# Kernel tuning notes

Measured on AMD Instinct MI355X. Metric: run time of the kernel, lower is better.

## Reference

```python
import jax, jax.numpy as jnp
import numpy as np

K = 16          # nsample / knn k
GROUPS = 4      # GroupNorm groups
EPS = 1e-5


def setup_inputs() -> dict:
    key = jax.random.key(0)
    ks = jax.random.split(key, 10)
    B, N = 8, 2048
    x = jax.random.normal(ks[0], (B, 3, N), jnp.float32)
    f = x  # at first call features == coordinates
    w = lambda i, shape: jax.random.normal(ks[i], shape, jnp.float32) * 0.05
    return dict(
        x=x, f=f,
        # input_trans: Conv1d(3 -> 64)
        W_it=w(1, (64, 3)), b_it=jnp.zeros((64,), jnp.float32),
        # layer1: Conv2d(128 -> 128, bias=False) + GroupNorm(4, 128)
        W1=w(2, (128, 128)), gn_g=jnp.ones((128,), jnp.float32), gn_b=jnp.zeros((128,), jnp.float32),
        # mlp1: Conv2d(128->256), Conv2d(256->512)
        Wa=w(3, (256, 128)), ba=jnp.zeros((256,), jnp.float32),
        Wb=w(4, (512, 256)), bb=jnp.zeros((512,), jnp.float32),
        # mlp2: Conv1d(640->256), Conv1d(256->128)
        Wc=w(5, (256, 640)), bc=jnp.zeros((256,), jnp.float32),
        Wd=w(6, (128, 256)), bd=jnp.zeros((128,), jnp.float32),
        # mlp3: Conv1d(128->256), Conv1d(256->512)
        We=w(7, (256, 128)), be=jnp.zeros((256,), jnp.float32),
        Wf=w(8, (512, 256)), bf=jnp.zeros((512,), jnp.float32),
    )


def _knn_idx(x):
    # x: (B, 3, N) -> idx: (B, N, K) indices of K nearest neighbors (self-knn)
    coor = jnp.transpose(x, (0, 2, 1))                       # (B, N, 3)
    sq = jnp.sum(coor * coor, axis=-1)                        # (B, N)
    d = sq[:, :, None] + sq[:, None, :] - 2.0 * jnp.einsum('bnc,bmc->bnm', coor, coor)
    _, idx = jax.lax.top_k(-d, K)                             # smallest distances
    return idx


def _group_norm(y, gamma, beta):
    # y: (B, N, K, C); torch GroupNorm normalizes over (C/g, N, K) per (b, group)
    B, N, Kk, C = y.shape
    yg = y.reshape(B, N, Kk, GROUPS, C // GROUPS)
    mu = jnp.mean(yg, axis=(1, 2, 4), keepdims=True)
    var = jnp.var(yg, axis=(1, 2, 4), keepdims=True)
    yg = (yg - mu) * jax.lax.rsqrt(var + EPS)
    return yg.reshape(B, N, Kk, C) * gamma + beta


def reference(x, f, W_it, b_it, W1, gn_g, gn_b, Wa, ba, Wb, bb, Wc, bc, Wd, bd, We, be, Wf, bf):
    B, _, N = x.shape
    idx = _knn_idx(x)                                          # (B, N, K)

    # input_trans: 1x1 conv over channels, channels-last layout (B, N, C)
    h = jnp.einsum('bcn,oc->bno', f, W_it) + b_it              # (B, N, 64)

    # graph feature: gather neighbors, build [nb - h, h]
    nb = jax.vmap(lambda hb, ib: hb[ib])(h, idx)               # (B, N, K, 64)
    hq = h[:, :, None, :]                                       # (B, N, 1, 64)
    feat = jnp.concatenate([nb - hq, jnp.broadcast_to(hq, nb.shape)], axis=-1)  # (B, N, K, 128)

    # layer1: conv1x1 (no bias) + GroupNorm + LeakyReLU(0.2)
    y = jnp.einsum('bnkc,oc->bnko', feat, W1)                  # (B, N, K, 128)
    y = jax.nn.leaky_relu(_group_norm(y, gn_g, gn_b), 0.2)

    local_base = jnp.max(y, axis=2)                             # (B, N, 128)

    # mlp1 over edges, then max over K and global max over N
    g = jax.nn.relu(jnp.einsum('bnkc,oc->bnko', y, Wa) + ba)    # (B, N, K, 256)
    g = jax.nn.relu(jnp.einsum('bnkc,oc->bnko', g, Wb) + bb)    # (B, N, K, 512)
    gfeat = jnp.max(g, axis=2)                                  # (B, N, 512)
    gmax = jnp.max(gfeat, axis=1, keepdims=True)                # (B, 1, 512)

    cat = jnp.concatenate([local_base, jnp.broadcast_to(gmax, (B, N, 512))], axis=-1)  # (B, N, 640)

    lf = jax.nn.relu(jnp.einsum('bnc,oc->bno', cat, Wc) + bc)   # (B, N, 256)
    lf = jax.nn.relu(jnp.einsum('bnc,oc->bno', lf, Wd) + bd)    # (B, N, 128)

    gl = jax.nn.relu(jnp.einsum('bnc,oc->bno', lf, We) + be)    # (B, N, 256)
    gl = jax.nn.relu(jnp.einsum('bnc,oc->bno', gl, Wf) + bf)    # (B, N, 512)
    gl = jnp.max(gl, axis=1, keepdims=True)                     # (B, 1, 512)

    global_feat = jnp.transpose(gl, (0, 2, 1))                  # (B, 512, 1)
    local_feat = jnp.transpose(lf, (0, 2, 1))                   # (B, 128, N)
    return (global_feat, local_feat)
```

## Files before the change

### kernel.cpp

```cpp
#include <hip/hip_runtime.h>
#include <hip/hip_bf16.h>

#define BATCH 8
#define NPTS 2048
#define KNNK 16
#define CH 64
#define CF 128
#define CA 256
#define CB 512
#define CCAT 640
#define CC 256
#define CD 128
#define CE 256
#define CG 512
#define NGRP 4
#define EPSF 1e-5f
#define GF_OFF (BATCH*CG)
#define P 8
#define MROWS (P*KNNK)
#define TM 64

typedef __attribute__((ext_vector_type(8))) short short8v;
typedef __attribute__((ext_vector_type(4))) float f32x4;

__device__ inline short f2bf(float f) {
  __hip_bfloat16 h = __float2bfloat16(f);
  return *reinterpret_cast<short*>(&h);
}

#define LIDX(r, c, ROW) ((r)*(ROW) + ((c) ^ (((r)&7)<<3)))

__device__ inline void pack_dev(const float* __restrict__ W, short* __restrict__ Wp,
                                int O, int C, int ld, int tid) {
  int KS = C >> 5;
  int total = (O >> 4) * KS * 64;
  if (tid >= total) return;
  int l = tid & 63;
  int fs = tid >> 6;
  int nt = fs / KS, ks = fs - nt * KS;
  int o = nt * 16 + (l & 15);
  int c = ks * 32 + (l >> 4) * 8;
  const float* src = W + (size_t)o * ld + c;
  short8v v;
#pragma unroll
  for (int j = 0; j < 8; ++j) v[j] = f2bf(src[j]);
  *(short8v*)&Wp[(size_t)tid * 8] = v;
}

__global__ __launch_bounds__(256)
void k_prep(const float* __restrict__ f, const float* __restrict__ Wit,
            const float* __restrict__ bit, float* __restrict__ h,
            const float* __restrict__ W1, short* __restrict__ W1p,
            const float* __restrict__ Wa, short* __restrict__ Wap,
            const float* __restrict__ Wb, short* __restrict__ Wbp,
            const float* __restrict__ Wc, short* __restrict__ WcLp,
            const float* __restrict__ Wd, short* __restrict__ Wdp,
            const float* __restrict__ We, short* __restrict__ Wep,
            const float* __restrict__ Wf, short* __restrict__ Wfp) {
  int blk = blockIdx.x;
  if (blk < 4096) {
    int t = blk * 256 + threadIdx.x;
    int o = t & (CH - 1);
    int bn = t >> 6;
    int n = bn & (NPTS - 1);
    int b = bn >> 11;
    float f0 = f[(b*3 + 0)*NPTS + n];
    float f1 = f[(b*3 + 1)*NPTS + n];
    float f2 = f[(b*3 + 2)*NPTS + n];
    h[t] = f0*Wit[o*3+0] + f1*Wit[o*3+1] + f2*Wit[o*3+2] + bit[o];
  } else if (blk < 4104) pack_dev(W1, W1p, CF, CF, CF, (blk-4096)*256 + threadIdx.x);
  else if (blk < 4120) pack_dev(Wa, Wap, CA, CF, CF, (blk-4104)*256 + threadIdx.x);
  else if (blk < 4184) pack_dev(Wb, Wbp, CB, CA, CA, (blk-4120)*256 + threadIdx.x);
  else if (blk < 4200) pack_dev(Wc, WcLp, CC, CF, CCAT, (blk-4184)*256 + threadIdx.x);
  else if (blk < 4216) pack_dev(Wd, Wdp, CD, CC, CC, (blk-4200)*256 + threadIdx.x);
  else if (blk < 4232) pack_dev(We, Wep, CE, CD, CD, (blk-4216)*256 + threadIdx.x);
  else                 pack_dev(Wf, Wfp, CG, CE, CE, (blk-4232)*256 + threadIdx.x);
}

__global__ __launch_bounds__(512)
void k_knn(const float* __restrict__ x, int* __restrict__ idxout) {
  __shared__ float xs0[2112], xs1[2112], xs2[2112], sqs[2112];
  int blk = blockIdx.x;
  int b = blk >> 8;
  int n0 = (blk & 255) * 8;
  int t = threadIdx.x;
  for (int i = t; i < NPTS; i += 512) {
    float x0 = x[(b*3 + 0)*NPTS + i];
    float x1 = x[(b*3 + 1)*NPTS + i];
    float x2 = x[(b*3 + 2)*NPTS + i];
    int a = (i >> 5)*33 + (i & 31);
    xs0[a] = x0; xs1[a] = x1; xs2[a] = x2;
    sqs[a] = __fadd_rn(__fadd_rn(__fmul_rn(x0,x0), __fmul_rn(x1,x1)), __fmul_rn(x2,x2));
  }
  __syncthreads();
  int lane = t & 63, wv = t >> 6;
  int q = n0 + wv;
  int qa = (q >> 5)*33 + (q & 31);
  float qx = xs0[qa], qy = xs1[qa], qz = xs2[qa];
  float sqq = sqs[qa];
  float d[32];
  int base = lane * 32;
#pragma unroll
  for (int jj = 0; jj < 32; ++jj) {
    int a = lane*33 + jj;
    float mx = xs0[a], my = xs1[a], mz = xs2[a];
    float dot = __fadd_rn(__fadd_rn(__fmul_rn(qx,mx), __fmul_rn(qy,my)), __fmul_rn(qz,mz));
    d[jj] = __fsub_rn(__fadd_rn(sqq, sqs[a]), __fadd_rn(dot, dot));
  }
  const float FINF = __builtin_inff();
  float sv0 = d[0]; int si0 = base;
#pragma unroll
  for (int jj = 1; jj < 16; ++jj)
    if (d[jj] < sv0) { sv0 = d[jj]; si0 = base + jj; }
  float sv1 = d[16]; int si1 = base + 16;
#pragma unroll
  for (int jj = 17; jj < 32; ++jj)
    if (d[jj] < sv1) { sv1 = d[jj]; si1 = base + jj; }
  int gsel = 0;
#pragma unroll
  for (int r = 0; r < KNNK; ++r) {
    float v = sv0; int i = si0;
    if (sv1 < v || (sv1 == v && si1 < i)) { v = sv1; i = si1; }
#pragma unroll
    for (int off = 32; off > 0; off >>= 1) {
      float v2 = __shfl_xor(v, off);
      int   i2 = __shfl_xor(i, off);
      if (v2 < v || (v2 == v && i2 < i)) { v = v2; i = i2; }
    }
    if (lane == r) gsel = i;
    int rem = ((i >> 5) == lane) ? (i & 31) : 64;
    if (rem < 16) {
      float nv = FINF; int ni = 0x7fffffff;
#pragma unroll
      for (int jj = 0; jj < 16; ++jj) {
        float dv = (jj == rem) ? FINF : d[jj];
        d[jj] = dv;
        if (dv < nv) { nv = dv; ni = base + jj; }
      }
      sv0 = nv; si0 = ni;
    } else if (rem < 32) {
      float nv = FINF; int ni = 0x7fffffff;
#pragma unroll
      for (int jj = 16; jj < 32; ++jj) {
        float dv = (jj == rem) ? FINF : d[jj];
        d[jj] = dv;
        if (dv < nv) { nv = dv; ni = base + jj; }
      }
      sv1 = nv; si1 = ni;
    }
  }
  if (lane < KNNK) idxout[(size_t)(b*NPTS + q)*KNNK + lane] = gsel;
}

__device__ inline void stage_feat(short* featS, const float* __restrict__ h,
                                  const int* __restrict__ idx, int b, int n0, int t) {
  int r = t >> 1, cb = (t & 1) * 32;
  int p = r >> 4, kk = r & 15;
  int nbi = idx[(size_t)(b*NPTS + n0 + p)*KNNK + kk];
  const float* hq = h + (size_t)(b*NPTS + n0 + p)*CH;
  const float* hn = h + (size_t)(b*NPTS + nbi)*CH;
#pragma unroll
  for (int j = 0; j < 32; j += 8) {
    float4 q0 = *(const float4*)(hq + cb + j);
    float4 q1 = *(const float4*)(hq + cb + j + 4);
    float4 a0 = *(const float4*)(hn + cb + j);
    float4 a1 = *(const float4*)(hn + cb + j + 4);
    short8v dv, qv;
    dv[0]=f2bf(a0.x-q0.x); dv[1]=f2bf(a0.y-q0.y); dv[2]=f2bf(a0.z-q0.z); dv[3]=f2bf(a0.w-q0.w);
    dv[4]=f2bf(a1.x-q1.x); dv[5]=f2bf(a1.y-q1.y); dv[6]=f2bf(a1.z-q1.z); dv[7]=f2bf(a1.w-q1.w);
    qv[0]=f2bf(q0.x); qv[1]=f2bf(q0.y); qv[2]=f2bf(q0.z); qv[3]=f2bf(q0.w);
    qv[4]=f2bf(q1.x); qv[5]=f2bf(q1.y); qv[6]=f2bf(q1.z); qv[7]=f2bf(q1.w);
    *(short8v*)&featS[LIDX(r, cb + j, CF)] = dv;
    *(short8v*)&featS[LIDX(r, 64 + cb + j, CF)] = qv;
  }
}

__global__ __launch_bounds__(256, 2)
void k_stats(const float* __restrict__ h, const int* __restrict__ idx,
             const short* __restrict__ W1p, float* __restrict__ partials) {
  __shared__ short featS[MROWS*CF];
  int blk = blockIdx.x;
  int b = blk >> 8;
  int n0 = (blk & 255) * P;
  int t = threadIdx.x;
  stage_feat(featS, h, idx, b, n0, t);
  __syncthreads();
  int lane = t & 63, wv = t >> 6;
  int r16 = lane & 15, g8 = (lane >> 4) * 8;
  float s = 0.f, ss = 0.f;
#pragma unroll
  for (int mh = 0; mh < 2; ++mh) {
    short8v af[4][4];
#pragma unroll
    for (int mm = 0; mm < 4; ++mm)
#pragma unroll
      for (int ks = 0; ks < 4; ++ks)
        af[mm][ks] = *(const short8v*)&featS[LIDX((mh*4+mm)*16 + r16, ks*32 + g8, CF)];
#pragma unroll
    for (int n = 0; n < 2; ++n) {
      int nt = 2*wv + n;
      short8v bfr[4];
#pragma unroll
      for (int ks = 0; ks < 4; ++ks)
        bfr[ks] = *(const short8v*)&W1p[(size_t)((nt*4 + ks)*64 + lane)*8];
#pragma unroll
      for (int mm = 0; mm < 4; ++mm) {
        f32x4 acc = {0.f, 0.f, 0.f, 0.f};
#pragma unroll
        for (int ks = 0; ks < 4; ++ks)
          acc = __builtin_amdgcn_mfma_f32_16x16x32_bf16(af[mm][ks], bfr[ks], acc, 0, 0, 0);
#pragma unroll
        for (int i = 0; i < 4; ++i) { s += acc[i]; ss += acc[i]*acc[i]; }
      }
    }
  }
#pragma unroll
  for (int off = 32; off > 0; off >>= 1) {
    s += __shfl_xor(s, off);
    ss += __shfl_xor(ss, off);
  }
  if (lane == 0) {
    partials[(size_t)(blk*NGRP + wv)*2 + 0] = s;
    partials[(size_t)(blk*NGRP + wv)*2 + 1] = ss;
  }
}

__global__ void k_reduce(const float* __restrict__ partials, float* __restrict__ stats) {
  int b = blockIdx.x >> 2, g = blockIdx.x & 3;
  int t = threadIdx.x;
  float s  = partials[(size_t)((b*256 + t)*NGRP + g)*2 + 0];
  float ss = partials[(size_t)((b*256 + t)*NGRP + g)*2 + 1];
  __shared__ float rs[256], rss[256];
  rs[t] = s; rss[t] = ss;
  __syncthreads();
  for (int st = 128; st > 0; st >>= 1) {
    if (t < st) { rs[t] += rs[t+st]; rss[t] += rss[t+st]; }
    __syncthreads();
  }
  if (t == 0) {
    const float cnt = (float)((size_t)NPTS * KNNK * 32);
    float mu = rs[0] / cnt;
    float var = rss[0] / cnt - mu*mu;
    stats[(b*NGRP+g)*2+0] = mu;
    stats[(b*NGRP+g)*2+1] = rsqrtf(var + EPSF);
  }
}

__global__ __launch_bounds__(256, 2)
void k_main(const float* __restrict__ h, const int* __restrict__ idx,
            const short* __restrict__ W1p, const float* __restrict__ gng,
            const float* __restrict__ gnb, const float* __restrict__ stats,
            const short* __restrict__ Wap, const float* __restrict__ ba,
            const short* __restrict__ Wbp, const float* __restrict__ bb,
            float* __restrict__ lbase, unsigned* __restrict__ gmaxU) {
  __shared__ short lds[MROWS*CA];
  short* featS = lds;
  short* ynS   = lds + MROWS*CF;
  short* g1S   = lds;
  int blk = blockIdx.x;
  int b = blk >> 8;
  int n0 = (blk & 255) * P;
  int t = threadIdx.x;
  stage_feat(featS, h, idx, b, n0, t);
  __syncthreads();
  int lane = t & 63, wv = t >> 6;
  int r16 = lane & 15, g8 = (lane >> 4) * 8;
  int rowg = (lane >> 4) * 4;
  {
    short8v af[8][4];
#pragma unroll
    for (int m = 0; m < 8; ++m)
#pragma unroll
      for (int ks = 0; ks < 4; ++ks)
        af[m][ks] = *(const short8v*)&featS[LIDX(m*16 + r16, ks*32 + g8, CF)];
    float mu  = stats[(b*NGRP + wv)*2 + 0];
    float rsg = stats[(b*NGRP + wv)*2 + 1];
#pragma unroll
    for (int n = 0; n < 2; ++n) {
      int nt = 2*wv + n;
      int o = nt*16 + r16;
      short8v bfr[4];
#pragma unroll
      for (int ks = 0; ks < 4; ++ks)
        bfr[ks] = *(const short8v*)&W1p[(size_t)((nt*4 + ks)*64 + lane)*8];
      float ga = gng[o], bev = gnb[o];
#pragma unroll
      for (int m = 0; m < 8; ++m) {
        f32x4 acc = {0.f, 0.f, 0.f, 0.f};
#pragma unroll
        for (int ks = 0; ks < 4; ++ks)
          acc = __builtin_amdgcn_mfma_f32_16x16x32_bf16(af[m][ks], bfr[ks], acc, 0, 0, 0);
        float vmax = -3.0e38f;
#pragma unroll
        for (int i = 0; i < 4; ++i) {
          float v = (acc[i] - mu) * rsg * ga + bev;
          v = (v >= 0.f) ? v : 0.2f*v;
          vmax = fmaxf(vmax, v);
          ynS[LIDX(m*16 + rowg + i, o, CF)] = f2bf(v);
        }
        vmax = fmaxf(vmax, __shfl_xor(vmax, 16));
        vmax = fmaxf(vmax, __shfl_xor(vmax, 32));
        if (lane < 16) lbase[(size_t)(b*NPTS + n0 + m)*CF + o] = vmax;
      }
    }
  }
  __syncthreads();
  {
    short8v yf[8][4];
#pragma unroll
    for (int m = 0; m < 8; ++m)
#pragma unroll
      for (int ks = 0; ks < 4; ++ks)
        yf[m][ks] = *(const short8v*)&ynS[LIDX(m*16 + r16, ks*32 + g8, CF)];
    __syncthreads();
#pragma unroll
    for (int nn = 0; nn < 4; ++nn) {
      int nt = wv*4 + nn;
      int o = nt*16 + r16;
      short8v bfr[4];
#pragma unroll
      for (int ks = 0; ks < 4; ++ks)
        bfr[ks] = *(const short8v*)&Wap[(size_t)((nt*4 + ks)*64 + lane)*8];
      float bav = ba[o];
#pragma unroll
      for (int m = 0; m < 8; ++m) {
        f32x4 acc = {0.f, 0.f, 0.f, 0.f};
#pragma unroll
        for (int ks = 0; ks < 4; ++ks)
          acc = __builtin_amdgcn_mfma_f32_16x16x32_bf16(yf[m][ks], bfr[ks], acc, 0, 0, 0);
#pragma unroll
        for (int i = 0; i < 4; ++i) {
          float v = fmaxf(acc[i] + bav, 0.f);
          g1S[LIDX(m*16 + rowg + i, o, CA)] = f2bf(v);
        }
      }
    }
  }
  __syncthreads();
#pragma unroll
  for (int half = 0; half < 2; ++half) {
    f32x4 acc[4][8];
#pragma unroll
    for (int nn = 0; nn < 4; ++nn)
#pragma unroll
      for (int m = 0; m < 8; ++m) acc[nn][m] = (f32x4){0.f, 0.f, 0.f, 0.f};
#pragma unroll
    for (int ks = 0; ks < 8; ++ks) {
      short8v gfk[8];
#pragma unroll
      for (int m = 0; m < 8; ++m)
        gfk[m] = *(const short8v*)&g1S[LIDX(m*16 + r16, ks*32 + g8, CA)];
#pragma unroll
      for (int nn = 0; nn < 4; ++nn) {
        int nt = wv*8 + half*4 + nn;
        short8v bfr = *(const short8v*)&Wbp[(size_t)((nt*8 + ks)*64 + lane)*8];
#pragma unroll
        for (int m = 0; m < 8; ++m)
          acc[nn][m] = __builtin_amdgcn_mfma_f32_16x16x32_bf16(gfk[m], bfr, acc[nn][m], 0, 0, 0);
      }
    }
#pragma unroll
    for (int nn = 0; nn < 4; ++nn) {
      int nt = wv*8 + half*4 + nn;
      float b0 = bb[nt*16 + r16];
      float am = 0.f;
#pragma unroll
      for (int m = 0; m < 8; ++m)
#pragma unroll
        for (int i = 0; i < 4; ++i) am = fmaxf(am, acc[nn][m][i] + b0);
      am = fmaxf(am, __shfl_xor(am, 16));
      am = fmaxf(am, __shfl_xor(am, 32));
      if (lane < 16) atomicMax(&gmaxU[b*CG + nt*16 + lane], __float_as_uint(am));
    }
  }
}

__global__ __launch_bounds__(256)
void k_gbias(const unsigned* __restrict__ gmaxU, const float* __restrict__ Wc,
             const float* __restrict__ bc, float* __restrict__ bceff) {
  __shared__ float gs[CB];
  int blk = blockIdx.x;
  int b = blk >> 5, og = blk & 31;
  int t = threadIdx.x;
  int lane = t & 63, wv = t >> 6;
  for (int i = t; i < CB; i += 256) gs[i] = __uint_as_float(gmaxU[b*CG + i]);
  __syncthreads();
#pragma unroll
  for (int j = 0; j < 2; ++j) {
    int o = og*8 + wv*2 + j;
    float acc = 0.f;
#pragma unroll
    for (int c8 = 0; c8 < 8; ++c8) {
      int c = lane + c8*64;
      acc += gs[c] * Wc[(size_t)o*CCAT + CF + c];
    }
#pragma unroll
    for (int off = 32; off > 0; off >>= 1) acc += __shfl_xor(acc, off);
    if (lane == 0) bceff[b*CC + o] = bc[o] + acc;
  }
}

__global__ __launch_bounds__(256)
void k_tail(const float* __restrict__ lbase, const float* __restrict__ bceff,
            const short* __restrict__ WcLp,
            const short* __restrict__ Wdp, const float* __restrict__ bd,
            const short* __restrict__ Wep, const float* __restrict__ be,
            const short* __restrict__ Wfp, const float* __restrict__ bf,
            float* __restrict__ out, unsigned* __restrict__ glmaxU) {
  __shared__ short aS0[TM*CF];
  __shared__ short aS1[TM*CA];
  int blk = blockIdx.x;
  int b = blk >> 5;
  int n0 = (blk & 31) * TM;
  int t = threadIdx.x;
  {
    int r = t >> 2, cb = (t & 3) * 32;
    const float* src = lbase + (size_t)(b*NPTS + n0 + r)*CF + cb;
#pragma unroll
    for (int j = 0; j < 32; j += 8) {
      float4 v0 = *(const float4*)(src + j);
      float4 v1 = *(const float4*)(src + j + 4);
      short8v pv;
      pv[0]=f2bf(v0.x); pv[1]=f2bf(v0.y); pv[2]=f2bf(v0.z); pv[3]=f2bf(v0.w);
      pv[4]=f2bf(v1.x); pv[5]=f2bf(v1.y); pv[6]=f2bf(v1.z); pv[7]=f2bf(v1.w);
      *(short8v*)&aS0[LIDX(r, cb + j, CF)] = pv;
    }
  }
  __syncthreads();
  int lane = t & 63, wv = t >> 6;
  int r16 = lane & 15, g8 = (lane >> 4) * 8;
  int rowg = (lane >> 4) * 4;
  {
    short8v af[4][4];
#pragma unroll
    for (int mt = 0; mt < 4; ++mt)
#pragma unroll
      for (int ks = 0; ks < 4; ++ks)
        af[mt][ks] = *(const short8v*)&aS0[LIDX(mt*16 + r16, ks*32 + g8, CF)];
#pragma unroll
    for (int nn = 0; nn < 4; ++nn) {
      int nt = wv*4 + nn;
      int o = nt*16 + r16;
      short8v bfr[4];
#pragma unroll
      for (int ks = 0; ks < 4; ++ks)
        bfr[ks] = *(const short8v*)&WcLp[(size_t)((nt*4 + ks)*64 + lane)*8];
      float bce = bceff[b*CC + o];
#pragma unroll
      for (int mt = 0; mt < 4; ++mt) {
        f32x4 acc = {0.f, 0.f, 0.f, 0.f};
#pragma unroll
        for (int ks = 0; ks < 4; ++ks)
          acc = __builtin_amdgcn_mfma_f32_16x16x32_bf16(af[mt][ks], bfr[ks], acc, 0, 0, 0);
#pragma unroll
        for (int i = 0; i < 4; ++i)
          aS1[LIDX(mt*16 + rowg + i, o, CA)] = f2bf(fmaxf(acc[i] + bce, 0.f));
      }
    }
  }
  __syncthreads();
  {
    short8v af[4][8];
#pragma unroll
    for (int mt = 0; mt < 4; ++mt)
#pragma unroll
      for (int ks = 0; ks < 8; ++ks)
        af[mt][ks] = *(const short8v*)&aS1[LIDX(mt*16 + r16, ks*32 + g8, CA)];
#pragma unroll
    for (int nn = 0; nn < 2; ++nn) {
      int nt = wv*2 + nn;
      int o = nt*16 + r16;
      short8v bfr[8];
#pragma unroll
      for (int ks = 0; ks < 8; ++ks)
        bfr[ks] = *(const short8v*)&Wdp[(size_t)((nt*8 + ks)*64 + lane)*8];
      float bdv = bd[o];
#pragma unroll
      for (int mt = 0; mt < 4; ++mt) {
        f32x4 acc = {0.f, 0.f, 0.f, 0.f};
#pragma unroll
        for (int ks = 0; ks < 8; ++ks)
          acc = __builtin_amdgcn_mfma_f32_16x16x32_bf16(af[mt][ks], bfr[ks], acc, 0, 0, 0);
#pragma unroll
        for (int i = 0; i < 4; ++i) {
          float v = fmaxf(acc[i] + bdv, 0.f);
          aS0[LIDX(mt*16 + rowg + i, o, CF)] = f2bf(v);
          out[GF_OFF + ((size_t)(b*CD + o))*NPTS + n0 + mt*16 + rowg + i] = v;
        }
      }
    }
  }
  __syncthreads();
  {
    short8v af[4][4];
#pragma unroll
    for (int mt = 0; mt < 4; ++mt)
#pragma unroll
      for (int ks = 0; ks < 4; ++ks)
        af[mt][ks] = *(const short8v*)&aS0[LIDX(mt*16 + r16, ks*32 + g8, CF)];
#pragma unroll
    for (int nn = 0; nn < 4; ++nn) {
      int nt = wv*4 + nn;
      int o = nt*16 + r16;
      short8v bfr[4];
#pragma unroll
      for (int ks = 0; ks < 4; ++ks)
        bfr[ks] = *(const short8v*)&Wep[(size_t)((nt*4 + ks)*64 + lane)*8];
      float bev = be[o];
#pragma unroll
      for (int mt = 0; mt < 4; ++mt) {
        f32x4 acc = {0.f, 0.f, 0.f, 0.f};
#pragma unroll
        for (int ks = 0; ks < 4; ++ks)
          acc = __builtin_amdgcn_mfma_f32_16x16x32_bf16(af[mt][ks], bfr[ks], acc, 0, 0, 0);
#pragma unroll
        for (int i = 0; i < 4; ++i)
          aS1[LIDX(mt*16 + rowg + i, o, CA)] = f2bf(fmaxf(acc[i] + bev, 0.f));
      }
    }
  }
  __syncthreads();
  {
    short8v af[4][8];
#pragma unroll
    for (int mt = 0; mt < 4; ++mt)
#pragma unroll
      for (int ks = 0; ks < 8; ++ks)
        af[mt][ks] = *(const short8v*)&aS1[LIDX(mt*16 + r16, ks*32 + g8, CA)];
#pragma unroll
    for (int nn = 0; nn < 8; ++nn) {
      int nt = wv*8 + nn;
      short8v bfr[8];
#pragma unroll
      for (int ks = 0; ks < 8; ++ks)
        bfr[ks] = *(const short8v*)&Wfp[(size_t)((nt*8 + ks)*64 + lane)*8];
      float bfv = bf[nt*16 + r16];
      float am = 0.f;
#pragma unroll
      for (int mt = 0; mt < 4; ++mt) {
        f32x4 acc = {0.f, 0.f, 0.f, 0.f};
#pragma unroll
        for (int ks = 0; ks < 8; ++ks)
          acc = __builtin_amdgcn_mfma_f32_16x16x32_bf16(af[mt][ks], bfr[ks], acc, 0, 0, 0);
#pragma unroll
        for (int i = 0; i < 4; ++i) am = fmaxf(am, acc[i] + bfv);
      }
      am = fmaxf(am, __shfl_xor(am, 16));
      am = fmaxf(am, __shfl_xor(am, 32));
      if (lane < 16) atomicMax(&glmaxU[b*CG + nt*16 + lane], __float_as_uint(am));
    }
  }
}

__global__ void k_final(const unsigned* __restrict__ glmaxU, float* __restrict__ out) {
  int i = blockIdx.x*256 + threadIdx.x;
  if (i < BATCH*CG) out[i] = __uint_as_float(glmaxU[i]);
}

extern "C" void kernel_launch(void* const* d_in, const int* in_sizes, int n_in,
                              void* d_out, int out_size, void* d_ws, size_t ws_size,
                              hipStream_t stream) {
  const float* x   = (const float*)d_in[0];
  const float* f   = (const float*)d_in[1];
  const float* Wit = (const float*)d_in[2];
  const float* bit = (const float*)d_in[3];
  const float* W1  = (const float*)d_in[4];
  const float* gng = (const float*)d_in[5];
  const float* gnb = (const float*)d_in[6];
  const float* Wa  = (const float*)d_in[7];
  const float* ba  = (const float*)d_in[8];
  const float* Wb  = (const float*)d_in[9];
  const float* bb  = (const float*)d_in[10];
  const float* Wc  = (const float*)d_in[11];
  const float* bc  = (const float*)d_in[12];
  const float* Wd  = (const float*)d_in[13];
  const float* bd  = (const float*)d_in[14];
  const float* We  = (const float*)d_in[15];
  const float* be  = (const float*)d_in[16];
  const float* Wf  = (const float*)d_in[17];
  const float* bf  = (const float*)d_in[18];
  float* out = (float*)d_out;

  char* w = (char*)d_ws;
  size_t off = 0;
  auto alloc = [&](size_t bytes) {
    void* p = w + off; off += (bytes + 255) & ~(size_t)255; return p;
  };
  float* h        = (float*)alloc((size_t)BATCH*NPTS*CH*4);
  int*   idx      = (int*)  alloc((size_t)BATCH*NPTS*KNNK*4);
  short* W1p      = (short*)alloc((size_t)CF*CF*2);
  short* Wap      = (short*)alloc((size_t)CA*CF*2);
  short* Wbp      = (short*)alloc((size_t)CB*CA*2);
  short* WcLp     = (short*)alloc((size_t)CC*CF*2);
  short* Wdp      = (short*)alloc((size_t)CD*CC*2);
  short* Wep      = (short*)alloc((size_t)CE*CD*2);
  short* Wfp      = (short*)alloc((size_t)CG*CE*2);
  float* bceff    = (float*)alloc((size_t)BATCH*CC*4);
  float* partials = (float*)alloc((size_t)(BATCH*NPTS/P)*NGRP*2*4);
  float* stats    = (float*)alloc((size_t)BATCH*NGRP*2*4);
  float* lbase    = (float*)alloc((size_t)BATCH*NPTS*CF*4);
  unsigned* gmaxU  = (unsigned*)alloc((size_t)BATCH*CG*4);
  unsigned* glmaxU = (unsigned*)alloc((size_t)BATCH*CG*4);

  hipMemsetAsync(gmaxU, 0, (size_t)BATCH*CG*4, stream);
  hipMemsetAsync(glmaxU, 0, (size_t)BATCH*CG*4, stream);

  k_prep<<<4296, 256, 0, stream>>>(f, Wit, bit, h, W1, W1p, Wa, Wap, Wb, Wbp,
                                   Wc, WcLp, Wd, Wdp, We, Wep, Wf, Wfp);
  k_knn<<<BATCH*NPTS/8, 512, 0, stream>>>(x, idx);
  k_stats<<<BATCH*NPTS/P, 256, 0, stream>>>(h, idx, W1p, partials);
  k_reduce<<<BATCH*NGRP, 256, 0, stream>>>(partials, stats);
  k_main<<<BATCH*NPTS/P, 256, 0, stream>>>(h, idx, W1p, gng, gnb, stats,
                                           Wap, ba, Wbp, bb, lbase, gmaxU);
  k_gbias<<<BATCH*32, 256, 0, stream>>>(gmaxU, Wc, bc, bceff);
  k_tail<<<BATCH*NPTS/TM, 256, 0, stream>>>(lbase, bceff, WcLp, Wdp, bd,
                                            Wep, be, Wfp, bf, out, glmaxU);
  k_final<<<(BATCH*CG+255)/256, 256, 0, stream>>>(glmaxU, out);
}
```

Baseline: 260.0 us.

## Fuse prep into knn kernel and fold gbias into tail with 512 threads

Merges the input-transform/weight-packing kernel into the kNN kernel as extra blocks, removing one launch. It also removes the separate global-bias kernel: each tail block recomputes its batch's effective conv bias from the global max into shared memory. k_tail moves to 512 threads (8 waves), with each wave taking fewer output tiles. The cost is redundant bias GEMV work in every tail block (32 blocks per batch), plus higher register/LDS pressure per block.

```diff
diff --git a/kernel.cpp b/kernel.cpp
--- a/kernel.cpp
+++ b/kernel.cpp
@@ -47,40 +47,39 @@
   *(short8v*)&Wp[(size_t)tid * 8] = v;
 }
 
-__global__ __launch_bounds__(256)
-void k_prep(const float* __restrict__ f, const float* __restrict__ Wit,
-            const float* __restrict__ bit, float* __restrict__ h,
-            const float* __restrict__ W1, short* __restrict__ W1p,
-            const float* __restrict__ Wa, short* __restrict__ Wap,
-            const float* __restrict__ Wb, short* __restrict__ Wbp,
-            const float* __restrict__ Wc, short* __restrict__ WcLp,
-            const float* __restrict__ Wd, short* __restrict__ Wdp,
-            const float* __restrict__ We, short* __restrict__ Wep,
-            const float* __restrict__ Wf, short* __restrict__ Wfp) {
+__global__ __launch_bounds__(512)
+void k_knn_prep(const float* __restrict__ x, int* __restrict__ idxout,
+                const float* __restrict__ f, const float* __restrict__ Wit,
+                const float* __restrict__ bit, float* __restrict__ h,
+                const float* __restrict__ W1, short* __restrict__ W1p,
+                const float* __restrict__ Wa, short* __restrict__ Wap,
+                const float* __restrict__ Wb, short* __restrict__ Wbp,
+                const float* __restrict__ Wc, short* __restrict__ WcLp,
+                const float* __restrict__ Wd, short* __restrict__ Wdp,
+                const float* __restrict__ We, short* __restrict__ Wep,
+                const float* __restrict__ Wf, short* __restrict__ Wfp) {
   int blk = blockIdx.x;
-  if (blk < 4096) {
-    int t = blk * 256 + threadIdx.x;
-    int o = t & (CH - 1);
-    int bn = t >> 6;
-    int n = bn & (NPTS - 1);
-    int b = bn >> 11;
-    float f0 = f[(b*3 + 0)*NPTS + n];
-    float f1 = f[(b*3 + 1)*NPTS + n];
-    float f2 = f[(b*3 + 2)*NPTS + n];
-    h[t] = f0*Wit[o*3+0] + f1*Wit[o*3+1] + f2*Wit[o*3+2] + bit[o];
-  } else if (blk < 4104) pack_dev(W1, W1p, CF, CF, CF, (blk-4096)*256 + threadIdx.x);
-  else if (blk < 4120) pack_dev(Wa, Wap, CA, CF, CF, (blk-4104)*256 + threadIdx.x);
-  else if (blk < 4184) pack_dev(Wb, Wbp, CB, CA, CA, (blk-4120)*256 + threadIdx.x);
-  else if (blk < 4200) pack_dev(Wc, WcLp, CC, CF, CCAT, (blk-4184)*256 + threadIdx.x);
-  else if (blk < 4216) pack_dev(Wd, Wdp, CD, CC, CC, (blk-4200)*256 + threadIdx.x);
-  else if (blk < 4232) pack_dev(We, Wep, CE, CD, CD, (blk-4216)*256 + threadIdx.x);
-  else                 pack_dev(Wf, Wfp, CG, CE, CE, (blk-4232)*256 + threadIdx.x);
-}
-
-__global__ __launch_bounds__(512)
-void k_knn(const float* __restrict__ x, int* __restrict__ idxout) {
+  if (blk >= 2048) {
+    if (blk < 4096) {
+      int t = (blk - 2048) * 512 + threadIdx.x;
+      int o = t & (CH - 1);
+      int bn = t >> 6;
+      int n = bn & (NPTS - 1);
+      int b = bn >> 11;
+      float f0 = f[(b*3 + 0)*NPTS + n];
+      float f1 = f[(b*3 + 1)*NPTS + n];
+      float f2 = f[(b*3 + 2)*NPTS + n];
+      h[t] = f0*Wit[o*3+0] + f1*Wit[o*3+1] + f2*Wit[o*3+2] + bit[o];
+    } else if (blk < 4100) pack_dev(W1, W1p, CF, CF, CF, (blk-4096)*512 + threadIdx.x);
+    else if (blk < 4108) pack_dev(Wa, Wap, CA, CF, CF, (blk-4100)*512 + threadIdx.x);
+    else if (blk < 4140) pack_dev(Wb, Wbp, CB, CA, CA, (blk-4108)*512 + threadIdx.x);
+    else if (blk < 4148) pack_dev(Wc, WcLp, CC, CF, CCAT, (blk-4140)*512 + threadIdx.x);
+    else if (blk < 4156) pack_dev(Wd, Wdp, CD, CC, CC, (blk-4148)*512 + threadIdx.x);
+    else if (blk < 4164) pack_dev(We, Wep, CE, CD, CD, (blk-4156)*512 + threadIdx.x);
+    else                 pack_dev(Wf, Wfp, CG, CE, CE, (blk-4164)*512 + threadIdx.x);
+    return;
+  }
   __shared__ float xs0[2112], xs1[2112], xs2[2112], sqs[2112];
-  int blk = blockIdx.x;
   int b = blk >> 8;
   int n0 = (blk & 255) * 8;
   int t = threadIdx.x;
@@ -375,33 +374,9 @@
   }
 }
 
-__global__ __launch_bounds__(256)
-void k_gbias(const unsigned* __restrict__ gmaxU, const float* __restrict__ Wc,
-             const float* __restrict__ bc, float* __restrict__ bceff) {
-  __shared__ float gs[CB];
-  int blk = blockIdx.x;
-  int b = blk >> 5, og = blk & 31;
-  int t = threadIdx.x;
-  int lane = t & 63, wv = t >> 6;
-  for (int i = t; i < CB; i += 256) gs[i] = __uint_as_float(gmaxU[b*CG + i]);
-  __syncthreads();
-#pragma unroll
-  for (int j = 0; j < 2; ++j) {
-    int o = og*8 + wv*2 + j;
-    float acc = 0.f;
-#pragma unroll
-    for (int c8 = 0; c8 < 8; ++c8) {
-      int c = lane + c8*64;
-      acc += gs[c] * Wc[(size_t)o*CCAT + CF + c];
-    }
-#pragma unroll
-    for (int off = 32; off > 0; off >>= 1) acc += __shfl_xor(acc, off);
-    if (lane == 0) bceff[b*CC + o] = bc[o] + acc;
-  }
-}
-
-__global__ __launch_bounds__(256)
-void k_tail(const float* __restrict__ lbase, const float* __restrict__ bceff,
+__global__ __launch_bounds__(512)
+void k_tail(const float* __restrict__ lbase, const unsigned* __restrict__ gmaxU,
+            const float* __restrict__ Wc, const float* __restrict__ bc,
             const short* __restrict__ WcLp,
             const short* __restrict__ Wdp, const float* __restrict__ bd,
             const short* __restrict__ Wep, const float* __restrict__ be,
@@ -409,25 +384,41 @@
             float* __restrict__ out, unsigned* __restrict__ glmaxU) {
   __shared__ short aS0[TM*CF];
   __shared__ short aS1[TM*CA];
+  __shared__ float bceffS[CC];
   int blk = blockIdx.x;
   int b = blk >> 5;
   int n0 = (blk & 31) * TM;
   int t = threadIdx.x;
-  {
-    int r = t >> 2, cb = (t & 3) * 32;
-    const float* src = lbase + (size_t)(b*NPTS + n0 + r)*CF + cb;
-#pragma unroll
-    for (int j = 0; j < 32; j += 8) {
+  int lane = t & 63, wv = t >> 6;
+  {
+    int r = t & 63, cs = (t >> 6) * 16;
+    const float* src = lbase + (size_t)(b*NPTS + n0 + r)*CF + cs;
+#pragma unroll
+    for (int j = 0; j < 16; j += 8) {
       float4 v0 = *(const float4*)(src + j);
       float4 v1 = *(const float4*)(src + j + 4);
       short8v pv;
       pv[0]=f2bf(v0.x); pv[1]=f2bf(v0.y); pv[2]=f2bf(v0.z); pv[3]=f2bf(v0.w);
       pv[4]=f2bf(v1.x); pv[5]=f2bf(v1.y); pv[6]=f2bf(v1.z); pv[7]=f2bf(v1.w);
-      *(short8v*)&aS0[LIDX(r, cb + j, CF)] = pv;
-    }
-  }
-  __syncthreads();
-  int lane = t & 63, wv = t >> 6;
+      *(short8v*)&aS0[LIDX(r, cs + j, CF)] = pv;
+    }
+  }
+  {
+    float gm[8];
+#pragma unroll
+    for (int k = 0; k < 8; ++k) gm[k] = __uint_as_float(gmaxU[b*CG + lane + 64*k]);
+    for (int j = 0; j < 32; ++j) {
+      int o = wv*32 + j;
+      const float* wrow = Wc + (size_t)o*CCAT + CF;
+      float acc = 0.f;
+#pragma unroll
+      for (int k = 0; k < 8; ++k) acc += gm[k] * wrow[lane + 64*k];
+#pragma unroll
+      for (int off = 32; off > 0; off >>= 1) acc += __shfl_xor(acc, off);
+      if (lane == 0) bceffS[o] = bc[o] + acc;
+    }
+  }
+  __syncthreads();
   int r16 = lane & 15, g8 = (lane >> 4) * 8;
   int rowg = (lane >> 4) * 4;
   {
@@ -438,14 +429,14 @@
       for (int ks = 0; ks < 4; ++ks)
         af[mt][ks] = *(const short8v*)&aS0[LIDX(mt*16 + r16, ks*32 + g8, CF)];
 #pragma unroll
-    for (int nn = 0; nn < 4; ++nn) {
-      int nt = wv*4 + nn;
+    for (int nn = 0; nn < 2; ++nn) {
+      int nt = wv*2 + nn;
       int o = nt*16 + r16;
       short8v bfr[4];
 #pragma unroll
       for (int ks = 0; ks < 4; ++ks)
         bfr[ks] = *(const short8v*)&WcLp[(size_t)((nt*4 + ks)*64 + lane)*8];
-      float bce = bceff[b*CC + o];
+      float bce = bceffS[o];
 #pragma unroll
       for (int mt = 0; mt < 4; ++mt) {
         f32x4 acc = {0.f, 0.f, 0.f, 0.f};
@@ -466,9 +457,8 @@
 #pragma unroll
       for (int ks = 0; ks < 8; ++ks)
         af[mt][ks] = *(const short8v*)&aS1[LIDX(mt*16 + r16, ks*32 + g8, CA)];
-#pragma unroll
-    for (int nn = 0; nn < 2; ++nn) {
-      int nt = wv*2 + nn;
+    {
+      int nt = wv;
       int o = nt*16 + r16;
       short8v bfr[8];
 #pragma unroll
@@ -499,37 +489,37 @@
       for (int ks = 0; ks < 4; ++ks)
         af[mt][ks] = *(const short8v*)&aS0[LIDX(mt*16 + r16, ks*32 + g8, CF)];
 #pragma unroll
+    for (int nn = 0; nn < 2; ++nn) {
+      int nt = wv*2 + nn;
+      int o = nt*16 + r16;
+      short8v bfr[4];
+#pragma unroll
+      for (int ks = 0; ks < 4; ++ks)
+        bfr[ks] = *(const short8v*)&Wep[(size_t)((nt*4 + ks)*64 + lane)*8];
+      float bev = be[o];
+#pragma unroll
+      for (int mt = 0; mt < 4; ++mt) {
+        f32x4 acc = {0.f, 0.f, 0.f, 0.f};
+#pragma unroll
+        for (int ks = 0; ks < 4; ++ks)
+          acc = __builtin_amdgcn_mfma_f32_16x16x32_bf16(af[mt][ks], bfr[ks], acc, 0, 0, 0);
+#pragma unroll
+        for (int i = 0; i < 4; ++i)
+          aS1[LIDX(mt*16 + rowg + i, o, CA)] = f2bf(fmaxf(acc[i] + bev, 0.f));
+      }
+    }
+  }
+  __syncthreads();
+  {
+    short8v af[4][8];
+#pragma unroll
+    for (int mt = 0; mt < 4; ++mt)
+#pragma unroll
+      for (int ks = 0; ks < 8; ++ks)
+        af[mt][ks] = *(const short8v*)&aS1[LIDX(mt*16 + r16, ks*32 + g8, CA)];
+#pragma unroll
     for (int nn = 0; nn < 4; ++nn) {
       int nt = wv*4 + nn;
-      int o = nt*16 + r16;
-      short8v bfr[4];
-#pragma unroll
-      for (int ks = 0; ks < 4; ++ks)
-        bfr[ks] = *(const short8v*)&Wep[(size_t)((nt*4 + ks)*64 + lane)*8];
-      float bev = be[o];
-#pragma unroll
-      for (int mt = 0; mt < 4; ++mt) {
-        f32x4 acc = {0.f, 0.f, 0.f, 0.f};
-#pragma unroll
-        for (int ks = 0; ks < 4; ++ks)
-          acc = __builtin_amdgcn_mfma_f32_16x16x32_bf16(af[mt][ks], bfr[ks], acc, 0, 0, 0);
-#pragma unroll
-        for (int i = 0; i < 4; ++i)
-          aS1[LIDX(mt*16 + rowg + i, o, CA)] = f2bf(fmaxf(acc[i] + bev, 0.f));
-      }
-    }
-  }
-  __syncthreads();
-  {
-    short8v af[4][8];
-#pragma unroll
-    for (int mt = 0; mt < 4; ++mt)
-#pragma unroll
-      for (int ks = 0; ks < 8; ++ks)
-        af[mt][ks] = *(const short8v*)&aS1[LIDX(mt*16 + r16, ks*32 + g8, CA)];
-#pragma unroll
-    for (int nn = 0; nn < 8; ++nn) {
-      int nt = wv*8 + nn;
       short8v bfr[8];
 #pragma unroll
       for (int ks = 0; ks < 8; ++ks)
@@ -595,7 +585,6 @@
   short* Wdp      = (short*)alloc((size_t)CD*CC*2);
   short* Wep      = (short*)alloc((size_t)CE*CD*2);
   short* Wfp      = (short*)alloc((size_t)CG*CE*2);
-  float* bceff    = (float*)alloc((size_t)BATCH*CC*4);
   float* partials = (float*)alloc((size_t)(BATCH*NPTS/P)*NGRP*2*4);
   float* stats    = (float*)alloc((size_t)BATCH*NGRP*2*4);
   float* lbase    = (float*)alloc((size_t)BATCH*NPTS*CF*4);
@@ -605,15 +594,14 @@
   hipMemsetAsync(gmaxU, 0, (size_t)BATCH*CG*4, stream);
   hipMemsetAsync(glmaxU, 0, (size_t)BATCH*CG*4, stream);
 
-  k_prep<<<4296, 256, 0, stream>>>(f, Wit, bit, h, W1, W1p, Wa, Wap, Wb, Wbp,
-                                   Wc, WcLp, Wd, Wdp, We, Wep, Wf, Wfp);
-  k_knn<<<BATCH*NPTS/8, 512, 0, stream>>>(x, idx);
+  k_knn_prep<<<4196, 512, 0, stream>>>(x, idx, f, Wit, bit, h, W1, W1p,
+                                       Wa, Wap, Wb, Wbp, Wc, WcLp,
+                                       Wd, Wdp, We, Wep, Wf, Wfp);
   k_stats<<<BATCH*NPTS/P, 256, 0, stream>>>(h, idx, W1p, partials);
   k_reduce<<<BATCH*NGRP, 256, 0, stream>>>(partials, stats);
   k_main<<<BATCH*NPTS/P, 256, 0, stream>>>(h, idx, W1p, gng, gnb, stats,
                                            Wap, ba, Wbp, bb, lbase, gmaxU);
-  k_gbias<<<BATCH*32, 256, 0, stream>>>(gmaxU, Wc, bc, bceff);
-  k_tail<<<BATCH*NPTS/TM, 256, 0, stream>>>(lbase, bceff, WcLp, Wdp, bd,
+  k_tail<<<BATCH*NPTS/TM, 512, 0, stream>>>(lbase, gmaxU, Wc, bc, WcLp, Wdp, bd,
                                             Wep, be, Wfp, bf, out, glmaxU);
   k_final<<<(BATCH*CG+255)/256, 256, 0, stream>>>(glmaxU, out);
 }
```

Measured after the change: 267.8 us. 3.0% more time.
